# Kernel tuning notes

Hardware: AMD Instinct MI355X
Metric: run time of the kernel (lower is better)

## Reference

```python
import jax, jax.numpy as jnp
import numpy as np
import math

B, S, H, DM, DFF = 8, 512, 16, 1024, 4096
DK = DM // H
EPS = 1e-6


def setup_inputs() -> dict:
    key = jax.random.key(0)
    ks = jax.random.split(key, 12)
    rn = lambda k, shape, s=0.02: (jax.random.normal(k, shape, jnp.float32) * s)
    return dict(
        x=jax.random.normal(ks[0], (B, S, DM), jnp.float32),
        mask=jnp.ones((B, 1, 1, S), jnp.int32),
        Wq=rn(ks[1], (DM, DM)), bq=jnp.zeros((DM,), jnp.float32),
        Wk=rn(ks[2], (DM, DM)), bk=jnp.zeros((DM,), jnp.float32),
        Wv=rn(ks[3], (DM, DM)), bv=jnp.zeros((DM,), jnp.float32),
        Wo=rn(ks[4], (DM, DM)), bo=jnp.zeros((DM,), jnp.float32),
        r_k=rn(ks[5], (S, S, DK)),
        r_v=rn(ks[6], (S, S, DK)),
        ln1_g=jnp.ones((DM,), jnp.float32), ln1_b=jnp.zeros((DM,), jnp.float32),
        ln2_g=jnp.ones((DM,), jnp.float32), ln2_b=jnp.zeros((DM,), jnp.float32),
        w1=rn(ks[7], (DFF, DM)), b1=jnp.zeros((DFF,), jnp.float32),
        w2=rn(ks[8], (DM, DFF)), b2=jnp.zeros((DM,), jnp.float32),
    )


def _layernorm(x, g, b):
    # torch: std with Bessel correction (ddof=1), divide by (std + eps)
    mean = jnp.mean(x, axis=-1, keepdims=True)
    std = jnp.std(x, axis=-1, keepdims=True, ddof=1)
    return g * (x - mean) / (std + EPS) + b


def _gelu_tanh(x):
    c = math.sqrt(2.0 / math.pi)
    return 0.5 * x * (1.0 + jnp.tanh(c * (x + 0.044715 * x * x * x)))


def _attention(xn, mask, Wq, bq, Wk, bk, Wv, bv, Wo, bo, r_k, r_v):
    def heads(x, W, bias):
        y = x @ W.T + bias                      # [B,S,DM]
        return y.reshape(B, S, H, DK).transpose(0, 2, 1, 3)  # [B,H,S,DK]
    q, k, v = heads(xn, Wq, bq), heads(xn, Wk, bk), heads(xn, Wv, bv)
    scale = 1.0 / math.sqrt(DK)
    scores = jnp.einsum('bhqd,bhkd->bhqk', q, k) * scale
    rel_score = jnp.einsum('bhqd,qkd->bhqk', q, r_k)  # relative-position bias
    scores = scores + rel_score * scale
    scores = jnp.where(mask == 0, -1e9, scores)
    p = jax.nn.softmax(scores, axis=-1)
    out = jnp.einsum('bhqk,bhkd->bhqd', p, v) + jnp.einsum('bhqk,qkd->bhqd', p, r_v)
    out = out.transpose(0, 2, 1, 3).reshape(B, S, DM)
    return out @ Wo.T + bo


def reference(x, mask, Wq, bq, Wk, bk, Wv, bv, Wo, bo, r_k, r_v,
              ln1_g, ln1_b, ln2_g, ln2_b, w1, b1, w2, b2):
    # sublayer 1: x + attn(LN(x))
    x = x + _attention(_layernorm(x, ln1_g, ln1_b), mask,
                       Wq, bq, Wk, bk, Wv, bv, Wo, bo, r_k, r_v)
    # sublayer 2: x + FFN(LN(x))
    h = _layernorm(x, ln2_g, ln2_b)
    h = _gelu_tanh(h @ w1.T + b1) @ w2.T + b2
    return x + h
```

## Files before the change

### kernel.cpp

```cpp
#include <hip/hip_runtime.h>
#include <math.h>


typedef unsigned short ushort_t;
typedef __attribute__((ext_vector_type(8))) short short8;
typedef __attribute__((ext_vector_type(4))) float f32x4;
typedef __attribute__((ext_vector_type(8))) __bf16 bf16x8;

__device__ __forceinline__ float b2f(ushort_t u) {
  unsigned v = (unsigned)u << 16;
  return __builtin_bit_cast(float, v);
}
__device__ __forceinline__ ushort_t f2b(float f) {
  unsigned x = __builtin_bit_cast(unsigned, f);
  x = x + 0x7fffu + ((x >> 16) & 1u);
  return (ushort_t)(x >> 16);
}

__device__ __forceinline__ void gload16(const ushort_t* g, ushort_t* l) {
  __builtin_amdgcn_global_load_lds(
      (const __attribute__((address_space(1))) unsigned*)g,
      (__attribute__((address_space(3))) unsigned*)l, 16, 0, 0);
}

__global__ void k_f32_to_bf16(const float* __restrict__ in,
                              ushort_t* __restrict__ out, long long n) {
  long long i = ((long long)blockIdx.x * blockDim.x + threadIdx.x) * 4;
  if (i >= n) return;
  float4 v = *reinterpret_cast<const float4*>(in + i);
  ushort4 o;
  o.x = f2b(v.x); o.y = f2b(v.y); o.z = f2b(v.z); o.w = f2b(v.w);
  *reinterpret_cast<ushort4*>(out + i) = o;
}

__global__ void k_layernorm_bf16(const float* __restrict__ x,
                                 const float* __restrict__ g,
                                 const float* __restrict__ b,
                                 ushort_t* __restrict__ out) {
  const int lane = threadIdx.x & 63;
  const int row = (blockIdx.x << 2) + (threadIdx.x >> 6);
  const float* xr = x + (long long)row * 1024;
  float4 v[4];
  float s = 0.f, ss = 0.f;
#pragma unroll
  for (int i = 0; i < 4; ++i) {
    v[i] = *reinterpret_cast<const float4*>(xr + lane * 16 + i * 4);
    s += v[i].x + v[i].y + v[i].z + v[i].w;
    ss += v[i].x * v[i].x + v[i].y * v[i].y + v[i].z * v[i].z + v[i].w * v[i].w;
  }
#pragma unroll
  for (int o = 32; o > 0; o >>= 1) {
    s += __shfl_xor(s, o);
    ss += __shfl_xor(ss, o);
  }
  float mean = s * (1.f / 1024.f);
  float var = (ss - 1024.f * mean * mean) * (1.f / 1023.f);
  var = fmaxf(var, 0.f);
  float inv = 1.f / (sqrtf(var) + 1e-6f);
  ushort_t* orow = out + (long long)row * 1024;
#pragma unroll
  for (int i = 0; i < 4; ++i) {
    int c = lane * 16 + i * 4;
    ushort4 o;
    o.x = f2b(g[c + 0] * (v[i].x - mean) * inv + b[c + 0]);
    o.y = f2b(g[c + 1] * (v[i].y - mean) * inv + b[c + 1]);
    o.z = f2b(g[c + 2] * (v[i].z - mean) * inv + b[c + 2]);
    o.w = f2b(g[c + 3] * (v[i].w - mean) * inv + b[c + 3]);
    *reinterpret_cast<ushort4*>(orow + c) = o;
  }
}

__global__ void k_softmax(ushort_t* __restrict__ sc, const int* __restrict__ mask,
                          float scale) {
  const int lane = threadIdx.x & 63;
  const long long row = ((long long)blockIdx.x << 2) + (threadIdx.x >> 6);
  const int b = (int)(row >> 13);
  ushort_t* srow = sc + row * 512;
  const int* mrow = mask + b * 512;
  short8 sv = *reinterpret_cast<const short8*>(srow + lane * 8);
  float vals[8];
  float mx = -1e30f;
#pragma unroll
  for (int j = 0; j < 8; ++j) {
    float f = b2f((ushort_t)sv[j]) * scale;
    if (mrow[lane * 8 + j] == 0) f = -1e9f;
    vals[j] = f;
    mx = fmaxf(mx, f);
  }
#pragma unroll
  for (int o = 32; o > 0; o >>= 1) mx = fmaxf(mx, __shfl_xor(mx, o));
  float s = 0.f;
#pragma unroll
  for (int j = 0; j < 8; ++j) {
    vals[j] = __expf(vals[j] - mx);
    s += vals[j];
  }
#pragma unroll
  for (int o = 32; o > 0; o >>= 1) s += __shfl_xor(s, o);
  float inv = 1.f / s;
  short8 ov;
#pragma unroll
  for (int j = 0; j < 8; ++j) ov[j] = (short)f2b(vals[j] * inv);
  *reinterpret_cast<short8*>(srow + lane * 8) = ov;
}

__global__ void k_transpose_v(const ushort_t* __restrict__ v,
                              ushort_t* __restrict__ vT) {
  __shared__ ushort_t tls[64][72];
  const int bh = blockIdx.y;
  const int s0 = blockIdx.x << 6;
  const int t = threadIdx.x;
  const long long base = (long long)bh * 32768;
#pragma unroll
  for (int it = 0; it < 2; ++it) {
    int r = (t >> 3) + it * 32;
    int c = (t & 7) << 3;
    short8 val = *reinterpret_cast<const short8*>(v + base + (long long)(s0 + r) * 64 + c);
    *reinterpret_cast<short8*>(&tls[r][c]) = val;
  }
  __syncthreads();
#pragma unroll
  for (int it = 0; it < 2; ++it) {
    int d = (t >> 3) + it * 32;
    int cs = (t & 7) << 3;
    short8 o;
#pragma unroll
    for (int j = 0; j < 8; ++j) o[j] = (short)tls[cs + j][d];
    *reinterpret_cast<short8*>(vT + base + (long long)d * 512 + s0 + cs) = o;
  }
}

__global__ void k_transpose_rv(const float* __restrict__ rv,
                               ushort_t* __restrict__ rvT) {
  __shared__ float tls[64][65];
  const int q = blockIdx.y;
  const int k0 = blockIdx.x << 6;
  const int t = threadIdx.x;
  const long long ibase = (long long)q * 32768;
#pragma unroll
  for (int it = 0; it < 4; ++it) {
    int r = (t >> 4) + it * 16;
    int c = (t & 15) << 2;
    float4 val = *reinterpret_cast<const float4*>(rv + ibase + (long long)(k0 + r) * 64 + c);
    tls[r][c] = val.x; tls[r][c + 1] = val.y; tls[r][c + 2] = val.z; tls[r][c + 3] = val.w;
  }
  __syncthreads();
#pragma unroll
  for (int it = 0; it < 2; ++it) {
    int d = (t >> 3) + it * 32;
    int cs = (t & 7) << 3;
    short8 o;
#pragma unroll
    for (int j = 0; j < 8; ++j) o[j] = (short)f2b(tls[cs + j][d]);
    *reinterpret_cast<short8*>(rvT + ibase + (long long)d * 512 + k0 + cs) = o;
  }
}

__global__ void k_reshape_attn(const ushort_t* __restrict__ a,
                               ushort_t* __restrict__ o) {
  long long i = (long long)blockIdx.x * 256 + threadIdx.x;
  int col8 = (int)(i & 127);
  long long tok = i >> 7;
  int col = col8 << 3;
  int h = col >> 6, d = col & 63;
  int bb = (int)(tok >> 9), s = (int)(tok & 511);
  short8 v = *reinterpret_cast<const short8*>(
      a + ((long long)(bb * 16 + h) * 512 + s) * 64 + d);
  *reinterpret_cast<short8*>(o + (tok << 10) + col) = v;
}

struct GArgs {
  const ushort_t* A; const ushort_t* B;
  long long a_bs, b_bs, c_bs;
  long long a_rs, b_rs, c_rs;
  int M, N, K;
  float scale;
  ushort_t* Cb;
  float* Cf;
  const float* bias;
  const float* resid;
  ushort_t* qb; ushort_t* kb; ushort_t* vb;
};

template <int MODE>
__global__ __launch_bounds__(256) void k_gemm_bt(GArgs g) {
  __shared__ ushort_t As[128 * 64];
  __shared__ ushort_t Bs[128 * 64];
  const int t = threadIdx.x;
  const int lane = t & 63;
  const int w = t >> 6, wr = w >> 1, wc = w & 1;
  const long long z = blockIdx.z;
  const int m0 = blockIdx.y * 128, n0 = blockIdx.x * 128;

  const ushort_t* Ab = g.A + z * g.a_bs;
  const ushort_t* Bb = g.B + z * g.b_bs;

  const int srow = t >> 3;
  const int scol = (((t & 7) ^ (srow & 7)) << 3);
  const ushort_t* Ap[4];
  const ushort_t* Bp[4];
#pragma unroll
  for (int p = 0; p < 4; ++p) {
    long long ar = min((long long)(m0 + p * 32 + srow), (long long)g.M - 1);
    long long br = min((long long)(n0 + p * 32 + srow), (long long)g.N - 1);
    Ap[p] = Ab + ar * g.a_rs + scol;
    Bp[p] = Bb + br * g.b_rs + scol;
  }

  f32x4 acc[4][4];
#pragma unroll
  for (int i = 0; i < 4; ++i)
#pragma unroll
    for (int j = 0; j < 4; ++j) acc[i][j] = f32x4{0.f, 0.f, 0.f, 0.f};

  const int fr = lane & 15;
  const int g4 = lane >> 4;
  const int fsw = fr & 7;

  const int nkt = g.K >> 6;
  for (int kt = 0; kt < nkt; ++kt) {
    const int k0 = kt << 6;
    __syncthreads();
#pragma unroll
    for (int p = 0; p < 4; ++p) {
      gload16(Ap[p] + k0, &As[p * 2048 + w * 512]);
      gload16(Bp[p] + k0, &Bs[p * 2048 + w * 512]);
    }
    __syncthreads();

    bf16x8 bfv[4][2];
#pragma unroll
    for (int j = 0; j < 4; ++j)
#pragma unroll
      for (int kk = 0; kk < 2; ++kk)
        bfv[j][kk] = *reinterpret_cast<const bf16x8*>(
            &Bs[(wc * 64 + j * 16 + fr) * 64 + (((kk * 4 + g4) ^ fsw) << 3)]);
#pragma unroll
    for (int i = 0; i < 4; ++i) {
      const int arow = (wr * 64 + i * 16 + fr) * 64;
      bf16x8 af0 = *reinterpret_cast<const bf16x8*>(
          &As[arow + ((g4 ^ fsw) << 3)]);
      bf16x8 af1 = *reinterpret_cast<const bf16x8*>(
          &As[arow + (((4 + g4) ^ fsw) << 3)]);
#pragma unroll
      for (int j = 0; j < 4; ++j) {
        acc[i][j] = __builtin_amdgcn_mfma_f32_16x16x32_bf16(af0, bfv[j][0],
                                                            acc[i][j], 0, 0, 0);
        acc[i][j] = __builtin_amdgcn_mfma_f32_16x16x32_bf16(af1, bfv[j][1],
                                                            acc[i][j], 0, 0, 0);
      }
    }
  }

  const int er0 = wr * 64 + (g4 << 2);
  const int ec0 = wc * 64 + fr;
#pragma unroll
  for (int i = 0; i < 4; ++i) {
#pragma unroll
    for (int j = 0; j < 4; ++j) {
#pragma unroll
      for (int r = 0; r < 4; ++r) {
        int row = m0 + er0 + i * 16 + r;
        int col = n0 + ec0 + j * 16;
        if (row >= g.M || col >= g.N) continue;
        float val = acc[i][j][r] * g.scale;
        if constexpr (MODE == 0) {
          g.Cb[z * g.c_bs + (long long)row * g.c_rs + col] = f2b(val);
        } else if constexpr (MODE == 1) {
          long long idx = z * g.c_bs + (long long)row * g.c_rs + col;
          g.Cb[idx] = f2b(b2f(g.Cb[idx]) + val);
        } else if constexpr (MODE == 2) {
          val += g.bias[col];
          int which = col >> 10;
          int h = (col >> 6) & 15;
          int d = col & 63;
          int bb = row >> 9, s = row & 511;
          ushort_t* dst = (which == 0) ? g.qb : (which == 1) ? g.kb : g.vb;
          dst[((long long)(bb * 16 + h) * 512 + s) * 64 + d] = f2b(val);
        } else if constexpr (MODE == 3) {
          long long idx = z * g.c_bs + (long long)row * g.c_rs + col;
          g.Cf[idx] = g.resid[idx] + val + g.bias[col];
        } else if constexpr (MODE == 4) {
          float xv = val + g.bias[col];
          float tv = tanhf(0.7978845608028654f * (xv + 0.044715f * xv * xv * xv));
          g.Cb[z * g.c_bs + (long long)row * g.c_rs + col] =
              f2b(0.5f * xv * (1.f + tv));
        }
      }
    }
  }
}

extern "C" void kernel_launch(void* const* d_in, const int* in_sizes, int n_in,
                              void* d_out, int out_size, void* d_ws,
                              size_t ws_size, hipStream_t stream) {
  const float* x    = (const float*)d_in[0];
  const int*   mask = (const int*)d_in[1];
  const float* Wq   = (const float*)d_in[2];
  const float* bq   = (const float*)d_in[3];
  const float* Wk   = (const float*)d_in[4];
  const float* bk   = (const float*)d_in[5];
  const float* Wv   = (const float*)d_in[6];
  const float* bv   = (const float*)d_in[7];
  const float* Wo   = (const float*)d_in[8];
  const float* bo   = (const float*)d_in[9];
  const float* r_k  = (const float*)d_in[10];
  const float* r_v  = (const float*)d_in[11];
  const float* ln1g = (const float*)d_in[12];
  const float* ln1b = (const float*)d_in[13];
  const float* ln2g = (const float*)d_in[14];
  const float* ln2b = (const float*)d_in[15];
  const float* w1   = (const float*)d_in[16];
  const float* b1   = (const float*)d_in[17];
  const float* w2   = (const float*)d_in[18];
  const float* b2   = (const float*)d_in[19];
  float* out = (float*)d_out;

  char* ws = (char*)d_ws;
  size_t off = 0;
  auto alloc = [&](size_t bytes) -> void* {
    void* p = ws + off;
    off += (bytes + 255) & ~(size_t)255;
    return p;
  };
  ushort_t* wqkv = (ushort_t*)alloc(3072ll * 1024 * 2);
  ushort_t* wo_b = (ushort_t*)alloc(1024ll * 1024 * 2);
  ushort_t* w1_b = (ushort_t*)alloc(4096ll * 1024 * 2);
  ushort_t* w2_b = (ushort_t*)alloc(1024ll * 4096 * 2);
  ushort_t* rk_b = (ushort_t*)alloc(512ll * 512 * 64 * 2);
  ushort_t* rvT  = (ushort_t*)alloc(512ll * 64 * 512 * 2);
  ushort_t* xn   = (ushort_t*)alloc(4096ll * 1024 * 2);
  ushort_t* qb   = (ushort_t*)alloc(128ll * 512 * 64 * 2);
  ushort_t* kb   = (ushort_t*)alloc(128ll * 512 * 64 * 2);
  ushort_t* vb   = (ushort_t*)alloc(128ll * 512 * 64 * 2);
  ushort_t* vT   = (ushort_t*)alloc(128ll * 64 * 512 * 2);
  ushort_t* scp  = (ushort_t*)alloc(128ll * 512 * 512 * 2);
  ushort_t* attn = (ushort_t*)alloc(128ll * 512 * 64 * 2);
  float*    x1   = (float*)alloc(4096ll * 1024 * 4);
  float*    bqkv = (float*)alloc(3072 * 4);
  ushort_t* attn_tok = xn;
  ushort_t* h_b = qb;
  ushort_t* mid = scp;

  hipMemcpyAsync(bqkv, bq, 1024 * 4, hipMemcpyDeviceToDevice, stream);
  hipMemcpyAsync(bqkv + 1024, bk, 1024 * 4, hipMemcpyDeviceToDevice, stream);
  hipMemcpyAsync(bqkv + 2048, bv, 1024 * 4, hipMemcpyDeviceToDevice, stream);

  auto cvt = [&](const float* src, ushort_t* dst, long long n) {
    k_f32_to_bf16<<<dim3((unsigned)((n / 4 + 255) / 256)), 256, 0, stream>>>(src, dst, n);
  };
  cvt(Wq, wqkv, 1024ll * 1024);
  cvt(Wk, wqkv + 1024ll * 1024, 1024ll * 1024);
  cvt(Wv, wqkv + 2048ll * 1024, 1024ll * 1024);
  cvt(Wo, wo_b, 1024ll * 1024);
  cvt(w1, w1_b, 4096ll * 1024);
  cvt(w2, w2_b, 1024ll * 4096);
  cvt(r_k, rk_b, 512ll * 512 * 64);
  k_transpose_rv<<<dim3(8, 512), 256, 0, stream>>>(r_v, rvT);

  k_layernorm_bf16<<<1024, 256, 0, stream>>>(x, ln1g, ln1b, xn);

  {
    GArgs a{};
    a.A = xn; a.B = wqkv; a.a_rs = 1024; a.b_rs = 1024;
    a.M = 4096; a.N = 3072; a.K = 1024; a.scale = 1.f;
    a.bias = bqkv; a.qb = qb; a.kb = kb; a.vb = vb;
    k_gemm_bt<2><<<dim3(24, 32, 1), 256, 0, stream>>>(a);
  }

  k_transpose_v<<<dim3(8, 128), 256, 0, stream>>>(vb, vT);

  {
    GArgs s{};
    s.A = qb; s.B = kb; s.a_bs = 32768; s.b_bs = 32768; s.c_bs = 262144;
    s.a_rs = 64; s.b_rs = 64; s.c_rs = 512;
    s.M = 512; s.N = 512; s.K = 64; s.scale = 1.f; s.Cb = scp;
    k_gemm_bt<0><<<dim3(4, 4, 128), 256, 0, stream>>>(s);
  }
  {
    GArgs r{};
    r.A = qb; r.B = rk_b; r.a_bs = 64; r.b_bs = 32768; r.c_bs = 512;
    r.a_rs = 32768; r.b_rs = 64; r.c_rs = 262144;
    r.M = 128; r.N = 512; r.K = 64; r.scale = 1.f; r.Cb = scp;
    k_gemm_bt<1><<<dim3(4, 1, 512), 256, 0, stream>>>(r);
  }

  k_softmax<<<16384, 256, 0, stream>>>(scp, mask, 0.125f);

  {
    GArgs pv{};
    pv.A = scp; pv.B = vT; pv.a_bs = 262144; pv.b_bs = 32768; pv.c_bs = 32768;
    pv.a_rs = 512; pv.b_rs = 512; pv.c_rs = 64;
    pv.M = 512; pv.N = 64; pv.K = 512; pv.scale = 1.f; pv.Cb = attn;
    k_gemm_bt<0><<<dim3(1, 4, 128), 256, 0, stream>>>(pv);
  }
  {
    GArgs pr{};
    pr.A = scp; pr.B = rvT; pr.a_bs = 512; pr.b_bs = 32768; pr.c_bs = 64;
    pr.a_rs = 262144; pr.b_rs = 512; pr.c_rs = 32768;
    pr.M = 128; pr.N = 64; pr.K = 512; pr.scale = 1.f; pr.Cb = attn;
    k_gemm_bt<1><<<dim3(1, 1, 512), 256, 0, stream>>>(pr);
  }

  k_reshape_attn<<<2048, 256, 0, stream>>>(attn, attn_tok);

  {
    GArgs o{};
    o.A = attn_tok; o.B = wo_b; o.a_rs = 1024; o.b_rs = 1024; o.c_rs = 1024;
    o.M = 4096; o.N = 1024; o.K = 1024; o.scale = 1.f;
    o.Cf = x1; o.bias = bo; o.resid = x;
    k_gemm_bt<3><<<dim3(8, 32, 1), 256, 0, stream>>>(o);
  }

  k_layernorm_bf16<<<1024, 256, 0, stream>>>(x1, ln2g, ln2b, h_b);

  {
    GArgs f1{};
    f1.A = h_b; f1.B = w1_b; f1.a_rs = 1024; f1.b_rs = 1024; f1.c_rs = 4096;
    f1.M = 4096; f1.N = 4096; f1.K = 1024; f1.scale = 1.f;
    f1.Cb = mid; f1.bias = b1;
    k_gemm_bt<4><<<dim3(32, 32, 1), 256, 0, stream>>>(f1);
  }
  {
    GArgs f2{};
    f2.A = mid; f2.B = w2_b; f2.a_rs = 4096; f2.b_rs = 4096; f2.c_rs = 1024;
    f2.M = 4096; f2.N = 1024; f2.K = 4096; f2.scale = 1.f;
    f2.Cf = out; f2.bias = b2; f2.resid = x1;
    k_gemm_bt<3><<<dim3(8, 32, 1), 256, 0, stream>>>(f2);
  }
}
```

Before: 649.4 us.

## Use register-direct wave-tiled GEMM without LDS for FFN1

Adds a GEMM kernel where each wave loads A and B fragments straight from global memory into registers, double-buffered across K steps. It skips LDS staging and uses a swizzled block-id mapping to group tiles for L2 locality. It is applied only to the FFN up-projection with fused GELU. The cost is no intra-block sharing of operands, so global and L2 traffic rises, and the fragment loads are narrow and strided rows.

```diff
diff --git a/kernel.cpp b/kernel.cpp
--- a/kernel.cpp
+++ b/kernel.cpp
@@ -291,6 +291,96 @@
   }
 }
 
+struct GW {
+  const ushort_t* A; const ushort_t* B;
+  long long a_rs, b_rs, c_rs;
+  int K;
+  ushort_t* Cb; float* Cf;
+  const float* bias; const float* resid;
+};
+
+template <int MODE>
+__global__ __launch_bounds__(256) void k_gemm_wave(GW g) {
+  const int t = threadIdx.x, lane = t & 63, w = t >> 6;
+  const int gx = gridDim.x;
+  int id = blockIdx.y * gx + blockIdx.x;
+  const int cpx = (gx * gridDim.y) >> 3;
+  id = (id & 7) * cpx + (id >> 3);
+  const int m0 = (id / gx) * 128 + (w >> 1) * 64;
+  const int n0 = (id % gx) * 128 + (w & 1) * 64;
+
+  const int fr = lane & 15, g4 = lane >> 4;
+  const ushort_t* Ab = g.A + (long long)(m0 + fr) * g.a_rs + g4 * 8;
+  const ushort_t* Bb = g.B + (long long)(n0 + fr) * g.b_rs + g4 * 8;
+  const long long a16 = 16 * g.a_rs, b16 = 16 * g.b_rs;
+
+  f32x4 acc[4][4];
+#pragma unroll
+  for (int i = 0; i < 4; ++i)
+#pragma unroll
+    for (int j = 0; j < 4; ++j) acc[i][j] = f32x4{0.f, 0.f, 0.f, 0.f};
+
+  bf16x8 a0[4], b0[4], a1[4], b1[4];
+#pragma unroll
+  for (int i = 0; i < 4; ++i) {
+    a0[i] = *reinterpret_cast<const bf16x8*>(Ab + i * a16);
+    b0[i] = *reinterpret_cast<const bf16x8*>(Bb + i * b16);
+  }
+
+  const int nkt = g.K >> 5;
+#pragma unroll 1
+  for (int kt = 0; kt < nkt; kt += 2) {
+    const int k1 = (kt + 1) << 5;
+#pragma unroll
+    for (int i = 0; i < 4; ++i) {
+      a1[i] = *reinterpret_cast<const bf16x8*>(Ab + i * a16 + k1);
+      b1[i] = *reinterpret_cast<const bf16x8*>(Bb + i * b16 + k1);
+    }
+#pragma unroll
+    for (int i = 0; i < 4; ++i)
+#pragma unroll
+      for (int j = 0; j < 4; ++j)
+        acc[i][j] = __builtin_amdgcn_mfma_f32_16x16x32_bf16(a0[i], b0[j],
+                                                            acc[i][j], 0, 0, 0);
+    if (kt + 2 < nkt) {
+      const int k2 = (kt + 2) << 5;
+#pragma unroll
+      for (int i = 0; i < 4; ++i) {
+        a0[i] = *reinterpret_cast<const bf16x8*>(Ab + i * a16 + k2);
+        b0[i] = *reinterpret_cast<const bf16x8*>(Bb + i * b16 + k2);
+      }
+    }
+#pragma unroll
+    for (int i = 0; i < 4; ++i)
+#pragma unroll
+      for (int j = 0; j < 4; ++j)
+        acc[i][j] = __builtin_amdgcn_mfma_f32_16x16x32_bf16(a1[i], b1[j],
+                                                            acc[i][j], 0, 0, 0);
+  }
+
+  const int er0 = g4 << 2;
+#pragma unroll
+  for (int i = 0; i < 4; ++i) {
+#pragma unroll
+    for (int j = 0; j < 4; ++j) {
+#pragma unroll
+      for (int r = 0; r < 4; ++r) {
+        const int row = m0 + er0 + i * 16 + r;
+        const int col = n0 + fr + j * 16;
+        float val = acc[i][j][r];
+        if constexpr (MODE == 3) {
+          long long idx = (long long)row * g.c_rs + col;
+          g.Cf[idx] = g.resid[idx] + val + g.bias[col];
+        } else if constexpr (MODE == 4) {
+          float xv = val + g.bias[col];
+          float tv = tanhf(0.7978845608028654f * (xv + 0.044715f * xv * xv * xv));
+          g.Cb[(long long)row * g.c_rs + col] = f2b(0.5f * xv * (1.f + tv));
+        }
+      }
+    }
+  }
+}
+
 extern "C" void kernel_launch(void* const* d_in, const int* in_sizes, int n_in,
                               void* d_out, int out_size, void* d_ws,
                               size_t ws_size, hipStream_t stream) {
@@ -415,11 +505,10 @@
   k_layernorm_bf16<<<1024, 256, 0, stream>>>(x1, ln2g, ln2b, h_b);
 
   {
-    GArgs f1{};
+    GW f1{};
     f1.A = h_b; f1.B = w1_b; f1.a_rs = 1024; f1.b_rs = 1024; f1.c_rs = 4096;
-    f1.M = 4096; f1.N = 4096; f1.K = 1024; f1.scale = 1.f;
-    f1.Cb = mid; f1.bias = b1;
-    k_gemm_bt<4><<<dim3(32, 32, 1), 256, 0, stream>>>(f1);
+    f1.K = 1024; f1.Cb = mid; f1.bias = b1;
+    k_gemm_wave<4><<<dim3(32, 32), 256, 0, stream>>>(f1);
   }
   {
     GArgs f2{};
```

After: 669.9 us. +3.2%, slower.

## Run FFN up-projection in FP8 and widen GEMM K-tile to 128

Applied to the files above, without the earlier changes.

Quantizes w1 (scaled by 64) and the second layernorm output to FP8 and computes the FFN first GEMM with a new FP8 MFMA kernel that fuses bias and GELU. The bf16 GEMM template gains a K-tile size parameter, set to 128 for the large GEMMs, which halves the number of barrier/load iterations. This trades numerical accuracy in the FFN for lower memory traffic and higher MFMA throughput, and uses more LDS per block.

```diff
diff --git a/kernel.cpp b/kernel.cpp
--- a/kernel.cpp
+++ b/kernel.cpp
@@ -3,6 +3,7 @@
 
 
 typedef unsigned short ushort_t;
+typedef unsigned char u8;
 typedef __attribute__((ext_vector_type(8))) short short8;
 typedef __attribute__((ext_vector_type(4))) float f32x4;
 typedef __attribute__((ext_vector_type(8))) __bf16 bf16x8;
@@ -18,6 +19,11 @@
 }
 
 __device__ __forceinline__ void gload16(const ushort_t* g, ushort_t* l) {
+  __builtin_amdgcn_global_load_lds(
+      (const __attribute__((address_space(1))) unsigned*)g,
+      (__attribute__((address_space(3))) unsigned*)l, 16, 0, 0);
+}
+__device__ __forceinline__ void gload16b(const u8* g, u8* l) {
   __builtin_amdgcn_global_load_lds(
       (const __attribute__((address_space(1))) unsigned*)g,
       (__attribute__((address_space(3))) unsigned*)l, 16, 0, 0);
@@ -31,6 +37,16 @@
   ushort4 o;
   o.x = f2b(v.x); o.y = f2b(v.y); o.z = f2b(v.z); o.w = f2b(v.w);
   *reinterpret_cast<ushort4*>(out + i) = o;
+}
+
+__global__ void k_f32_to_fp8(const float* __restrict__ in,
+                             u8* __restrict__ out, long long n, float scale) {
+  long long i = ((long long)blockIdx.x * blockDim.x + threadIdx.x) * 4;
+  if (i >= n) return;
+  float4 v = *reinterpret_cast<const float4*>(in + i);
+  int pk = __builtin_amdgcn_cvt_pk_fp8_f32(v.x * scale, v.y * scale, 0, false);
+  pk = __builtin_amdgcn_cvt_pk_fp8_f32(v.z * scale, v.w * scale, pk, true);
+  *reinterpret_cast<int*>(out + i) = pk;
 }
 
 __global__ void k_layernorm_bf16(const float* __restrict__ x,
@@ -67,6 +83,44 @@
     o.z = f2b(g[c + 2] * (v[i].z - mean) * inv + b[c + 2]);
     o.w = f2b(g[c + 3] * (v[i].w - mean) * inv + b[c + 3]);
     *reinterpret_cast<ushort4*>(orow + c) = o;
+  }
+}
+
+__global__ void k_layernorm_fp8(const float* __restrict__ x,
+                                const float* __restrict__ g,
+                                const float* __restrict__ b,
+                                u8* __restrict__ out) {
+  const int lane = threadIdx.x & 63;
+  const int row = (blockIdx.x << 2) + (threadIdx.x >> 6);
+  const float* xr = x + (long long)row * 1024;
+  float4 v[4];
+  float s = 0.f, ss = 0.f;
+#pragma unroll
+  for (int i = 0; i < 4; ++i) {
+    v[i] = *reinterpret_cast<const float4*>(xr + lane * 16 + i * 4);
+    s += v[i].x + v[i].y + v[i].z + v[i].w;
+    ss += v[i].x * v[i].x + v[i].y * v[i].y + v[i].z * v[i].z + v[i].w * v[i].w;
+  }
+#pragma unroll
+  for (int o = 32; o > 0; o >>= 1) {
+    s += __shfl_xor(s, o);
+    ss += __shfl_xor(ss, o);
+  }
+  float mean = s * (1.f / 1024.f);
+  float var = (ss - 1024.f * mean * mean) * (1.f / 1023.f);
+  var = fmaxf(var, 0.f);
+  float inv = 1.f / (sqrtf(var) + 1e-6f);
+  u8* orow = out + (long long)row * 1024;
+#pragma unroll
+  for (int i = 0; i < 4; ++i) {
+    int c = lane * 16 + i * 4;
+    float y0 = g[c + 0] * (v[i].x - mean) * inv + b[c + 0];
+    float y1 = g[c + 1] * (v[i].y - mean) * inv + b[c + 1];
+    float y2 = g[c + 2] * (v[i].z - mean) * inv + b[c + 2];
+    float y3 = g[c + 3] * (v[i].w - mean) * inv + b[c + 3];
+    int pk = __builtin_amdgcn_cvt_pk_fp8_f32(y0, y1, 0, false);
+    pk = __builtin_amdgcn_cvt_pk_fp8_f32(y2, y3, pk, true);
+    *reinterpret_cast<int*>(orow + c) = pk;
   }
 }
 
@@ -182,10 +236,14 @@
   ushort_t* qb; ushort_t* kb; ushort_t* vb;
 };
 
-template <int MODE>
+template <int MODE, int BKL>
 __global__ __launch_bounds__(256) void k_gemm_bt(GArgs g) {
-  __shared__ ushort_t As[128 * 64];
-  __shared__ ushort_t Bs[128 * 64];
+  constexpr int BKE = 1 << BKL;
+  constexpr int SLOTS = BKE / 8;
+  constexpr int RPP = 2048 / BKE;
+  constexpr int NPASS = 128 / RPP;
+  __shared__ ushort_t As[128 * BKE];
+  __shared__ ushort_t Bs[128 * BKE];
   const int t = threadIdx.x;
   const int lane = t & 63;
   const int w = t >> 6, wr = w >> 1, wc = w & 1;
@@ -195,14 +253,14 @@
   const ushort_t* Ab = g.A + z * g.a_bs;
   const ushort_t* Bb = g.B + z * g.b_bs;
 
-  const int srow = t >> 3;
-  const int scol = (((t & 7) ^ (srow & 7)) << 3);
-  const ushort_t* Ap[4];
-  const ushort_t* Bp[4];
-#pragma unroll
-  for (int p = 0; p < 4; ++p) {
-    long long ar = min((long long)(m0 + p * 32 + srow), (long long)g.M - 1);
-    long long br = min((long long)(n0 + p * 32 + srow), (long long)g.N - 1);
+  const int srow = t / SLOTS;
+  const int scol = (((t % SLOTS) ^ (srow & 7)) << 3);
+  const ushort_t* Ap[NPASS];
+  const ushort_t* Bp[NPASS];
+#pragma unroll
+  for (int p = 0; p < NPASS; ++p) {
+    long long ar = min((long long)(m0 + p * RPP + srow), (long long)g.M - 1);
+    long long br = min((long long)(n0 + p * RPP + srow), (long long)g.N - 1);
     Ap[p] = Ab + ar * g.a_rs + scol;
     Bp[p] = Bb + br * g.b_rs + scol;
   }
@@ -217,38 +275,34 @@
   const int g4 = lane >> 4;
   const int fsw = fr & 7;
 
-  const int nkt = g.K >> 6;
+  const int nkt = g.K >> BKL;
   for (int kt = 0; kt < nkt; ++kt) {
-    const int k0 = kt << 6;
+    const int k0 = kt << BKL;
     __syncthreads();
 #pragma unroll
-    for (int p = 0; p < 4; ++p) {
-      gload16(Ap[p] + k0, &As[p * 2048 + w * 512]);
-      gload16(Bp[p] + k0, &Bs[p * 2048 + w * 512]);
+    for (int p = 0; p < NPASS; ++p) {
+      gload16(Ap[p] + k0, &As[p * RPP * BKE + w * 512]);
+      gload16(Bp[p] + k0, &Bs[p * RPP * BKE + w * 512]);
     }
     __syncthreads();
 
-    bf16x8 bfv[4][2];
-#pragma unroll
-    for (int j = 0; j < 4; ++j)
-#pragma unroll
-      for (int kk = 0; kk < 2; ++kk)
-        bfv[j][kk] = *reinterpret_cast<const bf16x8*>(
-            &Bs[(wc * 64 + j * 16 + fr) * 64 + (((kk * 4 + g4) ^ fsw) << 3)]);
-#pragma unroll
-    for (int i = 0; i < 4; ++i) {
-      const int arow = (wr * 64 + i * 16 + fr) * 64;
-      bf16x8 af0 = *reinterpret_cast<const bf16x8*>(
-          &As[arow + ((g4 ^ fsw) << 3)]);
-      bf16x8 af1 = *reinterpret_cast<const bf16x8*>(
-          &As[arow + (((4 + g4) ^ fsw) << 3)]);
-#pragma unroll
-      for (int j = 0; j < 4; ++j) {
-        acc[i][j] = __builtin_amdgcn_mfma_f32_16x16x32_bf16(af0, bfv[j][0],
-                                                            acc[i][j], 0, 0, 0);
-        acc[i][j] = __builtin_amdgcn_mfma_f32_16x16x32_bf16(af1, bfv[j][1],
-                                                            acc[i][j], 0, 0, 0);
-      }
+#pragma unroll
+    for (int kk = 0; kk < BKE / 32; ++kk) {
+      bf16x8 av[4], bv[4];
+#pragma unroll
+      for (int j = 0; j < 4; ++j)
+        bv[j] = *reinterpret_cast<const bf16x8*>(
+            &Bs[(wc * 64 + j * 16 + fr) * BKE + (((kk * 4 + g4) ^ fsw) << 3)]);
+#pragma unroll
+      for (int i = 0; i < 4; ++i)
+        av[i] = *reinterpret_cast<const bf16x8*>(
+            &As[(wr * 64 + i * 16 + fr) * BKE + (((kk * 4 + g4) ^ fsw) << 3)]);
+#pragma unroll
+      for (int i = 0; i < 4; ++i)
+#pragma unroll
+        for (int j = 0; j < 4; ++j)
+          acc[i][j] = __builtin_amdgcn_mfma_f32_16x16x32_bf16(av[i], bv[j],
+                                                              acc[i][j], 0, 0, 0);
     }
   }
 
@@ -280,12 +334,94 @@
         } else if constexpr (MODE == 3) {
           long long idx = z * g.c_bs + (long long)row * g.c_rs + col;
           g.Cf[idx] = g.resid[idx] + val + g.bias[col];
-        } else if constexpr (MODE == 4) {
-          float xv = val + g.bias[col];
-          float tv = tanhf(0.7978845608028654f * (xv + 0.044715f * xv * xv * xv));
-          g.Cb[z * g.c_bs + (long long)row * g.c_rs + col] =
-              f2b(0.5f * xv * (1.f + tv));
         }
+      }
+    }
+  }
+}
+
+struct GF8 {
+  const u8* A; const u8* B;
+  long long a_rs, b_rs, c_rs;
+  int K;
+  ushort_t* Cb;
+  const float* bias;
+  float wscale;
+};
+
+__global__ __launch_bounds__(256) void k_gemm_f8(GF8 g) {
+  __shared__ u8 As[128 * 128];
+  __shared__ u8 Bs[128 * 128];
+  const int t = threadIdx.x;
+  const int lane = t & 63;
+  const int w = t >> 6, wr = w >> 1, wc = w & 1;
+  const int m0 = blockIdx.y * 128, n0 = blockIdx.x * 128;
+
+  const int srow = t >> 3;
+  const int scol = (((t & 7) ^ (srow & 7)) << 4);
+  const u8* Ap[4];
+  const u8* Bp[4];
+#pragma unroll
+  for (int p = 0; p < 4; ++p) {
+    Ap[p] = g.A + (long long)(m0 + p * 32 + srow) * g.a_rs + scol;
+    Bp[p] = g.B + (long long)(n0 + p * 32 + srow) * g.b_rs + scol;
+  }
+
+  f32x4 acc[4][4];
+#pragma unroll
+  for (int i = 0; i < 4; ++i)
+#pragma unroll
+    for (int j = 0; j < 4; ++j) acc[i][j] = f32x4{0.f, 0.f, 0.f, 0.f};
+
+  const int fr = lane & 15;
+  const int g4 = lane >> 4;
+  const int fsw = fr & 7;
+  const int bsel = (g4 & 1) * 8;
+
+  const int nkt = g.K >> 7;
+  for (int kt = 0; kt < nkt; ++kt) {
+    const int k0 = kt << 7;
+    __syncthreads();
+#pragma unroll
+    for (int p = 0; p < 4; ++p) {
+      gload16b(Ap[p] + k0, &As[(p * 32 + w * 8) * 128]);
+      gload16b(Bp[p] + k0, &Bs[(p * 32 + w * 8) * 128]);
+    }
+    __syncthreads();
+
+#pragma unroll
+    for (int ks = 0; ks < 4; ++ks) {
+      long long af[4], bf[4];
+#pragma unroll
+      for (int i = 0; i < 4; ++i) {
+        const int slot = ((ks * 2 + (g4 >> 1)) ^ fsw) << 4;
+        af[i] = *reinterpret_cast<const long long*>(
+            &As[(wr * 64 + i * 16 + fr) * 128 + slot + bsel]);
+        bf[i] = *reinterpret_cast<const long long*>(
+            &Bs[(wc * 64 + i * 16 + fr) * 128 + slot + bsel]);
+      }
+#pragma unroll
+      for (int i = 0; i < 4; ++i)
+#pragma unroll
+        for (int j = 0; j < 4; ++j)
+          acc[i][j] = __builtin_amdgcn_mfma_f32_16x16x32_fp8_fp8(
+              af[i], bf[j], acc[i][j], 0, 0, 0);
+    }
+  }
+
+  const int er0 = wr * 64 + (g4 << 2);
+  const int ec0 = wc * 64 + fr;
+#pragma unroll
+  for (int i = 0; i < 4; ++i) {
+#pragma unroll
+    for (int j = 0; j < 4; ++j) {
+#pragma unroll
+      for (int r = 0; r < 4; ++r) {
+        const int row = m0 + er0 + i * 16 + r;
+        const int col = n0 + ec0 + j * 16;
+        float xv = acc[i][j][r] * g.wscale + g.bias[col];
+        float tv = tanhf(0.7978845608028654f * (xv + 0.044715f * xv * xv * xv));
+        g.Cb[(long long)row * g.c_rs + col] = f2b(0.5f * xv * (1.f + tv));
       }
     }
   }
@@ -325,7 +461,7 @@
   };
   ushort_t* wqkv = (ushort_t*)alloc(3072ll * 1024 * 2);
   ushort_t* wo_b = (ushort_t*)alloc(1024ll * 1024 * 2);
-  ushort_t* w1_b = (ushort_t*)alloc(4096ll * 1024 * 2);
+  u8*       w1_8 = (u8*)alloc(4096ll * 1024);
   ushort_t* w2_b = (ushort_t*)alloc(1024ll * 4096 * 2);
   ushort_t* rk_b = (ushort_t*)alloc(512ll * 512 * 64 * 2);
   ushort_t* rvT  = (ushort_t*)alloc(512ll * 64 * 512 * 2);
@@ -339,7 +475,7 @@
   float*    x1   = (float*)alloc(4096ll * 1024 * 4);
   float*    bqkv = (float*)alloc(3072 * 4);
   ushort_t* attn_tok = xn;
-  ushort_t* h_b = qb;
+  u8* h_8 = (u8*)qb;
   ushort_t* mid = scp;
 
   hipMemcpyAsync(bqkv, bq, 1024 * 4, hipMemcpyDeviceToDevice, stream);
@@ -353,9 +489,9 @@
   cvt(Wk, wqkv + 1024ll * 1024, 1024ll * 1024);
   cvt(Wv, wqkv + 2048ll * 1024, 1024ll * 1024);
   cvt(Wo, wo_b, 1024ll * 1024);
-  cvt(w1, w1_b, 4096ll * 1024);
   cvt(w2, w2_b, 1024ll * 4096);
   cvt(r_k, rk_b, 512ll * 512 * 64);
+  k_f32_to_fp8<<<4096, 256, 0, stream>>>(w1, w1_8, 4096ll * 1024, 64.f);
   k_transpose_rv<<<dim3(8, 512), 256, 0, stream>>>(r_v, rvT);
 
   k_layernorm_bf16<<<1024, 256, 0, stream>>>(x, ln1g, ln1b, xn);
@@ -365,7 +501,7 @@
     a.A = xn; a.B = wqkv; a.a_rs = 1024; a.b_rs = 1024;
     a.M = 4096; a.N = 3072; a.K = 1024; a.scale = 1.f;
     a.bias = bqkv; a.qb = qb; a.kb = kb; a.vb = vb;
-    k_gemm_bt<2><<<dim3(24, 32, 1), 256, 0, stream>>>(a);
+    k_gemm_bt<2, 7><<<dim3(24, 32, 1), 256, 0, stream>>>(a);
   }
 
   k_transpose_v<<<dim3(8, 128), 256, 0, stream>>>(vb, vT);
@@ -375,14 +511,14 @@
     s.A = qb; s.B = kb; s.a_bs = 32768; s.b_bs = 32768; s.c_bs = 262144;
     s.a_rs = 64; s.b_rs = 64; s.c_rs = 512;
     s.M = 512; s.N = 512; s.K = 64; s.scale = 1.f; s.Cb = scp;
-    k_gemm_bt<0><<<dim3(4, 4, 128), 256, 0, stream>>>(s);
+    k_gemm_bt<0, 6><<<dim3(4, 4, 128), 256, 0, stream>>>(s);
   }
   {
     GArgs r{};
     r.A = qb; r.B = rk_b; r.a_bs = 64; r.b_bs = 32768; r.c_bs = 512;
     r.a_rs = 32768; r.b_rs = 64; r.c_rs = 262144;
     r.M = 128; r.N = 512; r.K = 64; r.scale = 1.f; r.Cb = scp;
-    k_gemm_bt<1><<<dim3(4, 1, 512), 256, 0, stream>>>(r);
+    k_gemm_bt<1, 6><<<dim3(4, 1, 512), 256, 0, stream>>>(r);
   }
 
   k_softmax<<<16384, 256, 0, stream>>>(scp, mask, 0.125f);
@@ -392,14 +528,14 @@
     pv.A = scp; pv.B = vT; pv.a_bs = 262144; pv.b_bs = 32768; pv.c_bs = 32768;
     pv.a_rs = 512; pv.b_rs = 512; pv.c_rs = 64;
     pv.M = 512; pv.N = 64; pv.K = 512; pv.scale = 1.f; pv.Cb = attn;
-    k_gemm_bt<0><<<dim3(1, 4, 128), 256, 0, stream>>>(pv);
+    k_gemm_bt<0, 7><<<dim3(1, 4, 128), 256, 0, stream>>>(pv);
   }
   {
     GArgs pr{};
     pr.A = scp; pr.B = rvT; pr.a_bs = 512; pr.b_bs = 32768; pr.c_bs = 64;
     pr.a_rs = 262144; pr.b_rs = 512; pr.c_rs = 32768;
     pr.M = 128; pr.N = 64; pr.K = 512; pr.scale = 1.f; pr.Cb = attn;
-    k_gemm_bt<1><<<dim3(1, 1, 512), 256, 0, stream>>>(pr);
+    k_gemm_bt<1, 7><<<dim3(1, 1, 512), 256, 0, stream>>>(pr);
   }
 
   k_reshape_attn<<<2048, 256, 0, stream>>>(attn, attn_tok);
@@ -409,23 +545,22 @@
     o.A = attn_tok; o.B = wo_b; o.a_rs = 1024; o.b_rs = 1024; o.c_rs = 1024;
     o.M = 4096; o.N = 1024; o.K = 1024; o.scale = 1.f;
     o.Cf = x1; o.bias = bo; o.resid = x;
-    k_gemm_bt<3><<<dim3(8, 32, 1), 256, 0, stream>>>(o);
-  }
-
-  k_layernorm_bf16<<<1024, 256, 0, stream>>>(x1, ln2g, ln2b, h_b);
-
-  {
-    GArgs f1{};
-    f1.A = h_b; f1.B = w1_b; f1.a_rs = 1024; f1.b_rs = 1024; f1.c_rs = 4096;
-    f1.M = 4096; f1.N = 4096; f1.K = 1024; f1.scale = 1.f;
-    f1.Cb = mid; f1.bias = b1;
-    k_gemm_bt<4><<<dim3(32, 32, 1), 256, 0, stream>>>(f1);
+    k_gemm_bt<3, 7><<<dim3(8, 32, 1), 256, 0, stream>>>(o);
+  }
+
+  k_layernorm_fp8<<<1024, 256, 0, stream>>>(x1, ln2g, ln2b, h_8);
+
+  {
+    GF8 f1{};
+    f1.A = h_8; f1.B = w1_8; f1.a_rs = 1024; f1.b_rs = 1024; f1.c_rs = 4096;
+    f1.K = 1024; f1.Cb = mid; f1.bias = b1; f1.wscale = 1.f / 64.f;
+    k_gemm_f8<<<dim3(32, 32), 256, 0, stream>>>(f1);
   }
   {
     GArgs f2{};
     f2.A = mid; f2.B = w2_b; f2.a_rs = 4096; f2.b_rs = 4096; f2.c_rs = 1024;
     f2.M = 4096; f2.N = 1024; f2.K = 4096; f2.scale = 1.f;
     f2.Cf = out; f2.bias = b2; f2.resid = x1;
-    k_gemm_bt<3><<<dim3(8, 32, 1), 256, 0, stream>>>(f2);
-  }
-}
+    k_gemm_bt<3, 7><<<dim3(8, 32, 1), 256, 0, stream>>>(f2);
+  }
+}
```

After: 606.9 us. 1.07x faster.
